# Kernel tuning notes

Measured on AMD Instinct MI355X. Metric: run time of the kernel, lower is better.

Reference implementation:

```python
import jax, jax.numpy as jnp
import numpy as np

HIDDEN = 512
HEADS = 8
HEAD_DIM = HIDDEN // HEADS
NUM_NODES = 512
NUM_EDGES = 16384
NEG_INF = -1e9


def setup_inputs() -> dict:
    key = jax.random.key(0)
    ks = jax.random.split(key, 8)
    x = jax.random.normal(ks[0], (4, 12, NUM_NODES, HIDDEN), dtype=jnp.float32)
    edge_index = jax.random.randint(ks[1], (2, NUM_EDGES), 0, NUM_NODES, dtype=jnp.int64)
    s = 1.0 / np.sqrt(HIDDEN)
    Wq = jax.random.uniform(ks[2], (HIDDEN, HIDDEN), jnp.float32, -s, s)
    Wk = jax.random.uniform(ks[3], (HIDDEN, HIDDEN), jnp.float32, -s, s)
    Wv = jax.random.uniform(ks[4], (HIDDEN, HIDDEN), jnp.float32, -s, s)
    bq = jax.random.uniform(ks[5], (HIDDEN,), jnp.float32, -s, s)
    bk = jax.random.uniform(ks[6], (HIDDEN,), jnp.float32, -s, s)
    bv = jax.random.uniform(ks[7], (HIDDEN,), jnp.float32, -s, s)
    return {"x": x, "edge_index": edge_index, "Wq": Wq, "bq": bq,
            "Wk": Wk, "bk": bk, "Wv": Wv, "bv": bv}


def reference(x, edge_index, Wq, bq, Wk, bk, Wv, bv):
    B, S, N, F = x.shape  # [batch, seq_len, num_nodes, features]
    xf = x.reshape(B * S, N, F)
    # torch nn.Linear: y = x @ W.T + b
    Q = xf @ Wq.T + bq
    K = xf @ Wk.T + bk
    V = xf @ Wv.T + bv
    # [B*S, heads, N, head_dim]
    Q = Q.reshape(B * S, N, HEADS, HEAD_DIM).transpose(0, 2, 1, 3)
    K = K.reshape(B * S, N, HEADS, HEAD_DIM).transpose(0, 2, 1, 3)
    V = V.reshape(B * S, N, HEADS, HEAD_DIM).transpose(0, 2, 1, 3)
    scores = jnp.einsum('bhnd,bhmd->bhnm', Q, K) / np.sqrt(HEAD_DIM)
    # static graph mask: 1 where edge exists
    mask = jnp.zeros((N, N), dtype=jnp.float32).at[edge_index[0], edge_index[1]].set(1.0)
    scores = jnp.where(mask[None, None] == 0, NEG_INF, scores)
    attn = jax.nn.softmax(scores, axis=-1)  # dropout is identity in eval
    out = jnp.einsum('bhnm,bhmd->bhnd', attn, V)
    out = out.transpose(0, 2, 1, 3).reshape(B, S, N, F)
    return out
```

## Files before the change

kernel.cpp:

```cpp
#include <hip/hip_runtime.h>
#include <hip/hip_bf16.h>

typedef __attribute__((ext_vector_type(8))) short short8;
typedef __attribute__((ext_vector_type(4))) float f32x4;
typedef __attribute__((ext_vector_type(4))) unsigned int u32x4;
typedef unsigned long long u64;
typedef unsigned short u16;
typedef unsigned int u32;

#define NODES 512
#define HIDDEN 512
#define NEDGES 16384

#define KOFF ((size_t)384 * 32 * 2 * 512)
#define VOFF ((size_t)2 * 384 * 32 * 2 * 512)

static __device__ __forceinline__ u16 f2bf(float f) {
  unsigned u = __float_as_uint(f);
  u += 0x7FFFu + ((u >> 16) & 1u);
  return (u16)(u >> 16);
}

static __device__ __forceinline__ void gld_lds16(const void* g, void* l) {
  __builtin_amdgcn_global_load_lds(
      (const __attribute__((address_space(1))) unsigned int*)g,
      (__attribute__((address_space(3))) unsigned int*)l, 16, 0, 0);
}

__global__ void cast_all(const float* __restrict__ x, const float* __restrict__ wq,
                         const float* __restrict__ wk, const float* __restrict__ wv,
                         u16* __restrict__ xb, u16* __restrict__ wb) {
  const int n4 = 3145728 + 196608;
  int stride = gridDim.x * blockDim.x;
  for (int i = blockIdx.x * blockDim.x + threadIdx.x; i < n4; i += stride) {
    if (i < 3145728) {
      float4 v = reinterpret_cast<const float4*>(x)[i];
      ushort4 o;
      o.x = f2bf(v.x); o.y = f2bf(v.y); o.z = f2bf(v.z); o.w = f2bf(v.w);
      reinterpret_cast<ushort4*>(xb)[i] = o;
    } else {
      int t = i - 3145728;
      int z = t >> 16;
      int wl = t & 65535;
      int jrow = wl >> 7;
      int k = (wl & 127) * 4;
      const float* src = (z == 0) ? wq : (z == 1) ? wk : wv;
      float4 v = reinterpret_cast<const float4*>(src)[wl];
      ushort4 o;
      o.x = f2bf(v.x); o.y = f2bf(v.y); o.z = f2bf(v.z); o.w = f2bf(v.w);
      size_t didx = (((size_t)(z * 32 + (jrow >> 4)) * 16 + (k >> 5)) * 64
                     + (((k >> 3) & 3) * 16 + (jrow & 15))) * 8 + (k & 7);
      *reinterpret_cast<ushort4*>(wb + didx) = o;
    }
  }
}

__global__ void mask_scatter(const int* __restrict__ e, u64* __restrict__ bits) {
  int i = blockIdx.x * blockDim.x + threadIdx.x;
  if (i < NEDGES) {
    int src = e[i];
    int dst = e[NEDGES + i];
    atomicOr(&bits[src * 8 + (dst >> 6)], 1ull << (dst & 63));
  }
}

__global__ void mask_frag(const u64* __restrict__ bits, u32* __restrict__ mf) {
  int idx = blockIdx.x * 256 + threadIdx.x;
  int w = idx & 3;
  int lane = (idx >> 2) & 63;
  int hh = (idx >> 8) & 1;
  int kt = (idx >> 9) & 7;
  int qsg = idx >> 12;
  int q = qsg * 16 + (lane & 15);
  int bit = hh * 32 + (lane >> 4) * 8 + 2 * w;
  u64 row = bits[q * 8 + kt];
  u32 b0 = (u32)(row >> bit) & 1u;
  u32 b1 = (u32)(row >> (bit + 1)) & 1u;
  mf[idx] = (b0 ? 0xFFFFu : 0u) | (b1 ? 0xFFFF0000u : 0u);
}

__global__ __launch_bounds__(256, 2)
void qkv_gemm(const u16* __restrict__ xb, const u16* __restrict__ wfrag,
              const float* __restrict__ bq, const float* __restrict__ bk,
              const float* __restrict__ bv, u16* __restrict__ qkv) {
  __shared__ u16 As[2][128 * 64];

  const int blk = blockIdx.x;
  const int xcd = blk & 7;
  const int i = blk >> 3;
  const int m0 = ((i % 24) + xcd * 24) * 128;
  const int nz = i / 24;
  const int n0 = (nz & 3) * 128;
  const int z = nz >> 2;

  const float* bias = (z == 0) ? bq : (z == 1) ? bk : bv;

  const int tid = threadIdx.x;
  const int lane = tid & 63;
  const int w = tid >> 6;
  const int wr = w >> 1, wc = w & 1;
  const int l = lane & 15, j = lane >> 4;
  const int sl = l & 7;
  const int kb = ((lane & 7) ^ (lane >> 3)) * 16;

  const u16* wf = wfrag + (((size_t)z * 32 + (n0 >> 4) + wc * 4) * 16) * 512 + lane * 8;

#define STAGE_A(bb, kt_) do {                                                   \
    const int k0_ = (kt_) * 64;                                                 \
    _Pragma("unroll")                                                           \
    for (int t_ = 0; t_ < 4; ++t_) {                                            \
      int c_ = w * 4 + t_;                                                      \
      int row_ = c_ * 8 + (lane >> 3);                                          \
      gld_lds16((const char*)xb + ((size_t)(m0 + row_) * 512 + k0_) * 2 + kb,   \
                (char*)&As[bb][0] + c_ * 1024);                                 \
    }                                                                           \
  } while (0)

  f32x4 acc[4][4] = {};

  STAGE_A(0, 0);
  int cur = 0;

  for (int kt = 0; kt < 8; ++kt) {
    short8 bf[4][2];
#pragma unroll
    for (int ni = 0; ni < 4; ++ni)
#pragma unroll
      for (int kk = 0; kk < 2; ++kk)
        bf[ni][kk] = *(const short8*)(wf + ((ni * 16) + (kt * 2 + kk)) * 512);

    if (kt < 7) {
      STAGE_A(cur ^ 1, kt + 1);
      asm volatile("s_waitcnt vmcnt(12)" ::: "memory");
    } else {
      asm volatile("s_waitcnt vmcnt(8)" ::: "memory");
    }
    __builtin_amdgcn_s_barrier();

#pragma unroll
    for (int kk = 0; kk < 2; ++kk) {
      short8 a[4];
#pragma unroll
      for (int mi = 0; mi < 4; ++mi)
        a[mi] = *(const short8*)(&As[cur][0] + (wr * 64 + mi * 16 + l) * 64 +
                                 (((kk * 4 + j) ^ sl) * 8));
      if (z == 2) {
#pragma unroll
        for (int mi = 0; mi < 4; ++mi)
#pragma unroll
          for (int ni = 0; ni < 4; ++ni)
            acc[mi][ni] = __builtin_amdgcn_mfma_f32_16x16x32_bf16(a[mi], bf[ni][kk], acc[mi][ni], 0, 0, 0);
      } else {
#pragma unroll
        for (int mi = 0; mi < 4; ++mi)
#pragma unroll
          for (int ni = 0; ni < 4; ++ni)
            acc[mi][ni] = __builtin_amdgcn_mfma_f32_16x16x32_bf16(bf[ni][kk], a[mi], acc[mi][ni], 0, 0, 0);
      }
    }

    if (kt < 7) {
      asm volatile("s_waitcnt lgkmcnt(0)" ::: "memory");
      __builtin_amdgcn_s_barrier();
    }
    cur ^= 1;
  }
#undef STAGE_A

  const int bs = m0 >> 9;
  const int hh = (n0 >> 6) + wc;
  const int bh = bs * 8 + hh;

  if (z == 2) {
    const int ktb = ((m0 & 511) >> 6) + wr;
#pragma unroll
    for (int ni = 0; ni < 4; ++ni) {
      int jcol = n0 + wc * 64 + ni * 16 + l;
      float bv_ = bias[jcol];
      int ds = ni;
#pragma unroll
      for (int mi = 0; mi < 4; ++mi) {
        int kk2 = mi >> 1, oct = ((mi & 1) << 1) | (j >> 1);
        ushort4 pk;
#pragma unroll
        for (int r = 0; r < 4; ++r) pk[r] = f2bf(acc[mi][ni][r] + bv_);
        size_t idx = VOFF + (((((size_t)bh * 8 + ktb) * 2 + kk2) * 4 + ds) * 512)
                   + (oct * 16 + l) * 8 + (j & 1) * 4;
        *reinterpret_cast<ushort4*>(qkv + idx) = pk;
      }
    }
  } else {
#pragma unroll
    for (int ni = 0; ni < 4; ++ni) {
      int n_base = n0 + wc * 64 + ni * 16 + j * 4;
      float4 b4 = *reinterpret_cast<const float4*>(bias + n_base);
      int kk = ni >> 1, oct = ((ni & 1) << 1) | (j >> 1);
#pragma unroll
      for (int mi = 0; mi < 4; ++mi) {
        ushort4 pk;
#pragma unroll
        for (int r = 0; r < 4; ++r) pk[r] = f2bf(acc[mi][ni][r] + (&b4.x)[r]);
        size_t idx;
        if (z == 0) {
          int qsg = ((m0 & 511) >> 4) + wr * 4 + mi;
          idx = ((((size_t)bh * 32 + qsg) * 2 + kk) * 512) + (oct * 16 + l) * 8 + (j & 1) * 4;
        } else {
          int ktb = ((m0 & 511) >> 6) + wr;
          idx = KOFF + (((((size_t)bh * 8 + ktb) * 4 + mi) * 2 + kk) * 512)
              + (oct * 16 + l) * 8 + (j & 1) * 4;
        }
        *reinterpret_cast<ushort4*>(qkv + idx) = pk;
      }
    }
  }
}

__global__ __launch_bounds__(256, 2)
void attn_kernel(const u16* __restrict__ qkv, const u32* __restrict__ mf,
                 float* __restrict__ out) {
  const int blk = blockIdx.x;
  const int xcd = blk & 7;
  const int i = blk >> 3;
  const int bh = xcd * 48 + (i >> 2);
  const int qq = i & 3;
  const int bs = bh >> 3, h = bh & 7;
  const int tid = threadIdx.x;
  const int lane = tid & 63;
  const int w = tid >> 6;
  const int l = lane & 15, j = lane >> 4;
  const int qb = qq * 8 + w * 2;

  short8 qf[2][2];
#pragma unroll
  for (int qs = 0; qs < 2; ++qs)
#pragma unroll
    for (int kk = 0; kk < 2; ++kk)
      qf[qs][kk] = *(const short8*)(qkv + (((size_t)bh * 32 + qb + qs) * 2 + kk) * 512 + lane * 8);

  const u16* Kp = qkv + KOFF + (size_t)bh * 32768 + lane * 8;
  const u16* Vp = qkv + VOFF + (size_t)bh * 32768 + lane * 8;
  const u32* M0 = mf + (qb + 0) * 4096 + lane * 4;
  const u32* M1 = mf + (qb + 1) * 4096 + lane * 4;

  f32x4 o[2][4] = {};
  f32x4 osum[2] = {};
  short8 ones;
#pragma unroll
  for (int t = 0; t < 8; ++t) ones[t] = (short)0x3F80;

#pragma unroll 1
  for (int p = 0; p < 16; ++p) {
    short8 kf2[2][2];
#pragma unroll
    for (int lks = 0; lks < 2; ++lks)
#pragma unroll
      for (int kk = 0; kk < 2; ++kk)
        kf2[lks][kk] = *(const short8*)(Kp + (lks * 2 + kk) * 512);
    short8 vf[4];
#pragma unroll
    for (int ds = 0; ds < 4; ++ds)
      vf[ds] = *(const short8*)(Vp + ds * 512);
    u32x4 am0 = *reinterpret_cast<const u32x4*>(M0);
    u32x4 am1 = *reinterpret_cast<const u32x4*>(M1);

#pragma unroll
    for (int qs = 0; qs < 2; ++qs) {
      f32x4 st[2] = {};
#pragma unroll
      for (int lks = 0; lks < 2; ++lks)
#pragma unroll
        for (int kk = 0; kk < 2; ++kk)
          st[lks] = __builtin_amdgcn_mfma_f32_16x16x32_bf16(
              kf2[lks][kk], qf[qs][kk], st[lks], 0, 0, 0);

      float pr[8];
#pragma unroll
      for (int lks = 0; lks < 2; ++lks)
#pragma unroll
        for (int r = 0; r < 4; ++r)
          pr[lks * 4 + r] = __builtin_exp2f(st[lks][r] * 0.18033688f);
      u32 X0, X1, Y0, Y1;
      asm("v_cvt_pk_bf16_f32 %0, %1, %2" : "=v"(X0) : "v"(pr[0]), "v"(pr[1]));
      asm("v_cvt_pk_bf16_f32 %0, %1, %2" : "=v"(X1) : "v"(pr[2]), "v"(pr[3]));
      asm("v_cvt_pk_bf16_f32 %0, %1, %2" : "=v"(Y0) : "v"(pr[4]), "v"(pr[5]));
      asm("v_cvt_pk_bf16_f32 %0, %1, %2" : "=v"(Y1) : "v"(pr[6]), "v"(pr[7]));
      asm("v_permlane32_swap_b32 %0, %1" : "+v"(X0), "+v"(Y0));
      asm("v_permlane32_swap_b32 %0, %1" : "+v"(X1), "+v"(Y1));
      asm("v_permlane16_swap_b32 %0, %1" : "+v"(X0), "+v"(Y0));
      asm("v_permlane16_swap_b32 %0, %1" : "+v"(X1), "+v"(Y1));
      const u32x4 am = qs ? am1 : am0;
      u32x4 paw;
      paw[0] = X0 & am[0];
      paw[1] = X1 & am[1];
      paw[2] = Y0 & am[2];
      paw[3] = Y1 & am[3];
      short8 pa = __builtin_bit_cast(short8, paw);
      osum[qs] = __builtin_amdgcn_mfma_f32_16x16x32_bf16(pa, ones, osum[qs], 0, 0, 0);
#pragma unroll
      for (int ds = 0; ds < 4; ++ds)
        o[qs][ds] = __builtin_amdgcn_mfma_f32_16x16x32_bf16(pa, vf[ds], o[qs][ds], 0, 0, 0);
    }

    Kp += 2048; Vp += 2048; M0 += 256; M1 += 256;
  }

#pragma unroll
  for (int qs = 0; qs < 2; ++qs) {
    f32x4 inv4;
#pragma unroll
    for (int r = 0; r < 4; ++r) inv4[r] = 1.0f / osum[qs][r];
#pragma unroll
    for (int ds = 0; ds < 4; ++ds) {
      int d = ds * 16 + l;
#pragma unroll
      for (int r = 0; r < 4; ++r) {
        int node = (qb + qs) * 16 + j * 4 + r;
        out[(size_t)bs * 262144 + (size_t)node * 512 + h * 64 + d] = o[qs][ds][r] * inv4[r];
      }
    }
  }
}

extern "C" void kernel_launch(void* const* d_in, const int* in_sizes, int n_in,
                              void* d_out, int out_size, void* d_ws, size_t ws_size,
                              hipStream_t stream) {
  const float* x  = (const float*)d_in[0];
  const int*   e  = (const int*)d_in[1];
  const float* Wq = (const float*)d_in[2];
  const float* bq = (const float*)d_in[3];
  const float* Wk = (const float*)d_in[4];
  const float* bk = (const float*)d_in[5];
  const float* Wv = (const float*)d_in[6];
  const float* bv = (const float*)d_in[7];
  float* out = (float*)d_out;

  char* ws = (char*)d_ws;
  u16* xb   = (u16*)(ws);
  u16* wb   = (u16*)(ws + 25165824);
  u16* qkv  = (u16*)(ws + 26738688);
  u64* mb   = (u64*)(ws + 102236160);
  u32* mfr  = (u32*)(ws + 102268928);

  hipMemsetAsync(mb, 0, 512 * 8 * sizeof(u64), stream);
  mask_scatter<<<(NEDGES + 255) / 256, 256, 0, stream>>>(e, mb);
  mask_frag<<<512, 256, 0, stream>>>(mb, mfr);

  cast_all<<<2048, 256, 0, stream>>>(x, Wq, Wk, Wv, xb, wb);

  qkv_gemm<<<2304, 256, 0, stream>>>(xb, wb, bq, bk, bv, qkv);
  attn_kernel<<<1536, 256, 0, stream>>>(qkv, mfr, out);
}
```

Measured before the change: 129.1 us.

## Fuse x fp32-to-bf16 cast into QKV GEMM A-tile loads

```diff
diff --git a/kernel.cpp b/kernel.cpp
--- a/kernel.cpp
+++ b/kernel.cpp
@@ -21,38 +21,20 @@
   return (u16)(u >> 16);
 }
 
-static __device__ __forceinline__ void gld_lds16(const void* g, void* l) {
-  __builtin_amdgcn_global_load_lds(
-      (const __attribute__((address_space(1))) unsigned int*)g,
-      (__attribute__((address_space(3))) unsigned int*)l, 16, 0, 0);
-}
-
-__global__ void cast_all(const float* __restrict__ x, const float* __restrict__ wq,
-                         const float* __restrict__ wk, const float* __restrict__ wv,
-                         u16* __restrict__ xb, u16* __restrict__ wb) {
-  const int n4 = 3145728 + 196608;
-  int stride = gridDim.x * blockDim.x;
-  for (int i = blockIdx.x * blockDim.x + threadIdx.x; i < n4; i += stride) {
-    if (i < 3145728) {
-      float4 v = reinterpret_cast<const float4*>(x)[i];
-      ushort4 o;
-      o.x = f2bf(v.x); o.y = f2bf(v.y); o.z = f2bf(v.z); o.w = f2bf(v.w);
-      reinterpret_cast<ushort4*>(xb)[i] = o;
-    } else {
-      int t = i - 3145728;
-      int z = t >> 16;
-      int wl = t & 65535;
-      int jrow = wl >> 7;
-      int k = (wl & 127) * 4;
-      const float* src = (z == 0) ? wq : (z == 1) ? wk : wv;
-      float4 v = reinterpret_cast<const float4*>(src)[wl];
-      ushort4 o;
-      o.x = f2bf(v.x); o.y = f2bf(v.y); o.z = f2bf(v.z); o.w = f2bf(v.w);
-      size_t didx = (((size_t)(z * 32 + (jrow >> 4)) * 16 + (k >> 5)) * 64
-                     + (((k >> 3) & 3) * 16 + (jrow & 15))) * 8 + (k & 7);
-      *reinterpret_cast<ushort4*>(wb + didx) = o;
-    }
-  }
+__global__ void cast_w(const float* __restrict__ wq, const float* __restrict__ wk,
+                       const float* __restrict__ wv, u16* __restrict__ wb) {
+  int t = blockIdx.x * 256 + threadIdx.x;
+  int z = t >> 16;
+  int wl = t & 65535;
+  int jrow = wl >> 7;
+  int k = (wl & 127) * 4;
+  const float* src = (z == 0) ? wq : (z == 1) ? wk : wv;
+  float4 v = reinterpret_cast<const float4*>(src)[wl];
+  ushort4 o;
+  o.x = f2bf(v.x); o.y = f2bf(v.y); o.z = f2bf(v.z); o.w = f2bf(v.w);
+  size_t didx = (((size_t)(z * 32 + (jrow >> 4)) * 16 + (k >> 5)) * 64
+                 + (((k >> 3) & 3) * 16 + (jrow & 15))) * 8 + (k & 7);
+  *reinterpret_cast<ushort4*>(wb + didx) = o;
 }
 
 __global__ void mask_scatter(const int* __restrict__ e, u64* __restrict__ bits) {
@@ -80,7 +62,7 @@
 }
 
 __global__ __launch_bounds__(256, 2)
-void qkv_gemm(const u16* __restrict__ xb, const u16* __restrict__ wfrag,
+void qkv_gemm(const float* __restrict__ x, const u16* __restrict__ wfrag,
               const float* __restrict__ bq, const float* __restrict__ bk,
               const float* __restrict__ bv, u16* __restrict__ qkv) {
   __shared__ u16 As[2][128 * 64];
@@ -88,10 +70,10 @@
   const int blk = blockIdx.x;
   const int xcd = blk & 7;
   const int i = blk >> 3;
-  const int m0 = ((i % 24) + xcd * 24) * 128;
-  const int nz = i / 24;
-  const int n0 = (nz & 3) * 128;
-  const int z = nz >> 2;
+  const int m0 = (xcd * 24 + i / 12) * 128;
+  const int r12 = i % 12;
+  const int z = r12 >> 2;
+  const int n0 = (r12 & 3) * 128;
 
   const float* bias = (z == 0) ? bq : (z == 1) ? bk : bv;
 
@@ -101,24 +83,42 @@
   const int wr = w >> 1, wc = w & 1;
   const int l = lane & 15, j = lane >> 4;
   const int sl = l & 7;
-  const int kb = ((lane & 7) ^ (lane >> 3)) * 16;
+  const int rs = lane >> 3;
+  const int cc = lane & 7;
 
   const u16* wf = wfrag + (((size_t)z * 32 + (n0 >> 4) + wc * 4) * 16) * 512 + lane * 8;
 
-#define STAGE_A(bb, kt_) do {                                                   \
-    const int k0_ = (kt_) * 64;                                                 \
+#define LOAD_A(ar, kt_) do {                                                    \
     _Pragma("unroll")                                                           \
     for (int t_ = 0; t_ < 4; ++t_) {                                            \
-      int c_ = w * 4 + t_;                                                      \
-      int row_ = c_ * 8 + (lane >> 3);                                          \
-      gld_lds16((const char*)xb + ((size_t)(m0 + row_) * 512 + k0_) * 2 + kb,   \
-                (char*)&As[bb][0] + c_ * 1024);                                 \
+      const float* src_ = x + (size_t)(m0 + (w * 4 + t_) * 8 + rs) * 512        \
+                            + (kt_) * 64 + cc * 8;                              \
+      ar[t_][0] = *reinterpret_cast<const float4*>(src_);                       \
+      ar[t_][1] = *reinterpret_cast<const float4*>(src_ + 4);                   \
     }                                                                           \
   } while (0)
 
+#define WRITE_A(ar, bb) do {                                                    \
+    _Pragma("unroll")                                                           \
+    for (int t_ = 0; t_ < 4; ++t_) {                                            \
+      u32x4 dw_;                                                                \
+      asm("v_cvt_pk_bf16_f32 %0, %1, %2" : "=v"(dw_[0]) : "v"(ar[t_][0].x), "v"(ar[t_][0].y)); \
+      asm("v_cvt_pk_bf16_f32 %0, %1, %2" : "=v"(dw_[1]) : "v"(ar[t_][0].z), "v"(ar[t_][0].w)); \
+      asm("v_cvt_pk_bf16_f32 %0, %1, %2" : "=v"(dw_[2]) : "v"(ar[t_][1].x), "v"(ar[t_][1].y)); \
+      asm("v_cvt_pk_bf16_f32 %0, %1, %2" : "=v"(dw_[3]) : "v"(ar[t_][1].z), "v"(ar[t_][1].w)); \
+      *reinterpret_cast<u32x4*>(&As[bb][0] + ((w * 4 + t_) * 8 + rs) * 64 +     \
+                                ((cc ^ rs) * 8)) = dw_;                         \
+    }                                                                           \
+  } while (0)
+
   f32x4 acc[4][4] = {};
 
-  STAGE_A(0, 0);
+  {
+    float4 ar0[4][2];
+    LOAD_A(ar0, 0);
+    WRITE_A(ar0, 0);
+  }
+  __syncthreads();
   int cur = 0;
 
   for (int kt = 0; kt < 8; ++kt) {
@@ -129,13 +129,8 @@
       for (int kk = 0; kk < 2; ++kk)
         bf[ni][kk] = *(const short8*)(wf + ((ni * 16) + (kt * 2 + kk)) * 512);
 
-    if (kt < 7) {
-      STAGE_A(cur ^ 1, kt + 1);
-      asm volatile("s_waitcnt vmcnt(12)" ::: "memory");
-    } else {
-      asm volatile("s_waitcnt vmcnt(8)" ::: "memory");
-    }
-    __builtin_amdgcn_s_barrier();
+    float4 ar[4][2];
+    if (kt < 7) LOAD_A(ar, kt + 1);
 
 #pragma unroll
     for (int kk = 0; kk < 2; ++kk) {
@@ -159,13 +154,12 @@
       }
     }
 
-    if (kt < 7) {
-      asm volatile("s_waitcnt lgkmcnt(0)" ::: "memory");
-      __builtin_amdgcn_s_barrier();
-    }
+    if (kt < 7) WRITE_A(ar, cur ^ 1);
+    __syncthreads();
     cur ^= 1;
   }
-#undef STAGE_A
+#undef LOAD_A
+#undef WRITE_A
 
   const int bs = m0 >> 9;
   const int hh = (n0 >> 6) + wc;
@@ -335,18 +329,16 @@
   float* out = (float*)d_out;
 
   char* ws = (char*)d_ws;
-  u16* xb   = (u16*)(ws);
-  u16* wb   = (u16*)(ws + 25165824);
-  u16* qkv  = (u16*)(ws + 26738688);
-  u64* mb   = (u64*)(ws + 102236160);
-  u32* mfr  = (u32*)(ws + 102268928);
+  u16* wb   = (u16*)(ws);
+  u16* qkv  = (u16*)(ws + 1572864);
+  u64* mb   = (u64*)(ws + 77070336);
+  u32* mfr  = (u32*)(ws + 77103104);
 
   hipMemsetAsync(mb, 0, 512 * 8 * sizeof(u64), stream);
   mask_scatter<<<(NEDGES + 255) / 256, 256, 0, stream>>>(e, mb);
   mask_frag<<<512, 256, 0, stream>>>(mb, mfr);
-
-  cast_all<<<2048, 256, 0, stream>>>(x, Wq, Wk, Wv, xb, wb);
-
-  qkv_gemm<<<2304, 256, 0, stream>>>(xb, wb, bq, bk, bv, qkv);
+  cast_w<<<768, 256, 0, stream>>>(Wq, Wk, Wv, wb);
+
+  qkv_gemm<<<2304, 256, 0, stream>>>(x, wb, bq, bk, bv, qkv);
   attn_kernel<<<1536, 256, 0, stream>>>(qkv, mfr, out);
 }
```

New measurement: 130.9 us. About the same (+1.4%).
